# Performance work log

Hardware: AMD Instinct MI355X
Metric: run time of the kernel (lower is better)

The kernel has to match this reference:

```python
import jax, jax.numpy as jnp
import numpy as np
from jax import lax

HEADS = 8
DIM_HEAD = 8
SCALE = DIM_HEAD ** (-0.5)
UP = 64  # nn.Upsample(scale_factor=64), nearest


def _conv_s8(x, w, b):
    # Conv2d(inner, inner, 11x11, stride 8, padding 2) + exact GELU
    y = lax.conv_general_dilated(x, w, window_strides=(8, 8),
                                 padding=((2, 2), (2, 2)),
                                 dimension_numbers=('NCHW', 'OIHW', 'NCHW'))
    return jax.nn.gelu(y + b[None, :, None, None], approximate=False)


def setup_inputs() -> dict:
    key = jax.random.key(0)
    ks = jax.random.split(key, 8)
    b, c, h, w = 2, 64, 48, 48
    inner = HEADS * DIM_HEAD  # 64
    f = jax.random.normal(ks[0], (b, c, h, w), jnp.float32)
    w_qkv = jax.random.normal(ks[1], (inner * 3, c, 1, 1), jnp.float32) * 0.05
    wq = jax.random.normal(ks[2], (inner, inner, 11, 11), jnp.float32) * 0.02
    bq = jax.random.normal(ks[3], (inner,), jnp.float32) * 0.02
    wk = jax.random.normal(ks[4], (inner, inner, 11, 11), jnp.float32) * 0.02
    bk = jax.random.normal(ks[5], (inner,), jnp.float32) * 0.02
    pos_h = jax.random.normal(ks[6], (DIM_HEAD, h), jnp.float32) * SCALE
    pos_w = jax.random.normal(ks[7], (DIM_HEAD, w), jnp.float32) * SCALE
    return {"f": f, "w_qkv": w_qkv, "wq": wq, "bq": bq, "wk": wk,
            "bk": bk, "pos_h": pos_h, "pos_w": pos_w}


def reference(f, w_qkv, wq, bq, wk, bk, pos_h, pos_w):
    b, c, h, w = f.shape
    inner = HEADS * DIM_HEAD
    # 1x1 conv to qkv
    qkv = jnp.einsum('oc,bchw->bohw', w_qkv[:, :, 0, 0], f)
    q, k, v = jnp.split(qkv, 3, axis=1)  # each [b, inner, h, w]
    # positional logits from pre-conv q
    q_full = q.reshape(b, HEADS, DIM_HEAD, h * w)
    emb = (pos_h[:, :, None] + pos_w[:, None, :]).reshape(DIM_HEAD, h * w)
    pos_logits = jnp.einsum('bhci,cj->bhij', q_full, emb)  # [b,H,hw,hw]
    # strided conv + gelu on q,k
    qd = _conv_s8(q, wq, bq)
    kd = _conv_s8(k, wk, bk)
    m = qd.shape[-1]  # downsampled side
    qd = qd.reshape(b, HEADS, DIM_HEAD, m * m) * SCALE
    kd = kd.reshape(b, HEADS, DIM_HEAD, m * m)
    vv = v.reshape(b, HEADS, DIM_HEAD, h * w)
    dots = jnp.einsum('bhci,bhcj->bhij', qd, kd)  # [b,H,m^2,m^2]
    # nearest upsample x64 on last two dims
    dots = jnp.repeat(jnp.repeat(dots, UP, axis=-2), UP, axis=-1)
    attn = jax.nn.softmax(dots + pos_logits, axis=-1)
    fmap = jnp.einsum('bhij,bhcj->bhci', attn, vv)
    return fmap.reshape(b, inner, h, w)
```

## Files before the change

### kernel.cpp

```cpp
#include <hip/hip_runtime.h>
#include <math.h>

#define HW 2304
#define O192 192
#define SCALE_F 0.35355339059327373f

typedef unsigned int u32;
typedef __attribute__((address_space(1))) const u32 gu32;
typedef __attribute__((address_space(3))) u32 lu32;
__device__ __forceinline__ void dma16(const void* g, void* l) {
  __builtin_amdgcn_global_load_lds((gu32*)g, (lu32*)l, 16, 0, 0);
}

__global__ __launch_bounds__(256) void qkv_kernel(
    const float* __restrict__ F, const float* __restrict__ W,
    float* __restrict__ QKV, float* __restrict__ V2) {
  __shared__ __align__(16) float sW[384];
  int blk = blockIdx.x;
  int idx0 = blk * 256;
  int r0 = idx0 / HW;
  int r1 = (idx0 + 255) / HW;
  int tid = threadIdx.x;
  if (tid < 192) {
    int g = tid >> 6, c = tid & 63;
    sW[tid]       = W[((r0 & 63) + g * 64) * 64 + c];
    sW[192 + tid] = W[((r1 & 63) + g * 64) * 64 + c];
  }
  __syncthreads();
  int idx = idx0 + tid;
  int p  = idx % HW;
  int r  = idx / HW;
  int o0 = r & 63;
  int b  = r >> 6;
  const float4* w4 = (const float4*)(sW + ((r == r0) ? 0 : 192));
  const float* f = F + (b * 64) * HW + p;
  float aq = 0.f, ak = 0.f, av = 0.f;
  #pragma unroll 4
  for (int c4 = 0; c4 < 16; c4++) {
    float4 wq = w4[c4];
    float4 wk = w4[16 + c4];
    float4 wv = w4[32 + c4];
    float f0 = f[(c4 * 4 + 0) * HW];
    float f1 = f[(c4 * 4 + 1) * HW];
    float f2 = f[(c4 * 4 + 2) * HW];
    float f3 = f[(c4 * 4 + 3) * HW];
    aq = fmaf(wq.x, f0, aq); ak = fmaf(wk.x, f0, ak); av = fmaf(wv.x, f0, av);
    aq = fmaf(wq.y, f1, aq); ak = fmaf(wk.y, f1, ak); av = fmaf(wv.y, f1, av);
    aq = fmaf(wq.z, f2, aq); ak = fmaf(wk.z, f2, ak); av = fmaf(wv.z, f2, av);
    aq = fmaf(wq.w, f3, aq); ak = fmaf(wk.w, f3, ak); av = fmaf(wv.w, f3, av);
  }
  float* qp = QKV + (b * HW + p) * O192;
  qp[o0]      = aq;
  qp[o0 + 64] = ak;
  V2[(((b << 3) + (o0 >> 3)) * HW + p) * 8 + (o0 & 7)] = av;
}

__global__ __launch_bounds__(256) void conv_kernel(
    const float* __restrict__ QKV, const float* __restrict__ Wq,
    const float* __restrict__ Bq, const float* __restrict__ Wk,
    const float* __restrict__ Bk, float* __restrict__ QD) {
  __shared__ float sW[7744];
  __shared__ float sRed[4 * 64 * 6];
  int blk = blockIdx.x;
  int xcd = blk & 7;
  int T = xcd >> 2, b = (xcd >> 1) & 1, s = xcd & 1;
  int idx = (blk >> 3) * 2 + s;
  int o  = idx / 6;
  int oy = idx % 6;
  const float* Wg = T ? Wk : Wq;
  for (int i = threadIdx.x; i < 7744; i += 256) sW[i] = Wg[o * 7744 + i];
  __syncthreads();
  int wv = threadIdx.x >> 6;
  int c  = threadIdx.x & 63;
  const float* base = QKV + b * (HW * O192) + T * 64 + c;
  float acc[6];
  #pragma unroll
  for (int ox = 0; ox < 6; ox++) acc[ox] = 0.f;
  for (int kyi = 0; kyi < 3; kyi++) {
    int ky = wv * 3 + kyi;
    if (ky > 10) break;
    int y = oy * 8 - 2 + ky;
    if ((unsigned)y < 48u) {
      float xrow[48];
      #pragma unroll
      for (int x = 0; x < 48; x++) xrow[x] = base[(y * 48 + x) * O192];
      #pragma unroll
      for (int kx = 0; kx < 11; kx++) {
        float wt = sW[c * 121 + ky * 11 + kx];
        #pragma unroll
        for (int ox = 0; ox < 6; ox++) {
          int x = ox * 8 - 2 + kx;
          if (x >= 0 && x < 48) acc[ox] = fmaf(xrow[x], wt, acc[ox]);
        }
      }
    }
  }
  #pragma unroll
  for (int ox = 0; ox < 6; ox++) sRed[(wv * 64 + c) * 6 + ox] = acc[ox];
  __syncthreads();
  if (threadIdx.x < 64) {
    int t = threadIdx.x;
    float r[6];
    #pragma unroll
    for (int ox = 0; ox < 6; ox++)
      r[ox] = sRed[t * 6 + ox] + sRed[(64 + t) * 6 + ox]
            + sRed[(128 + t) * 6 + ox] + sRed[(192 + t) * 6 + ox];
    #pragma unroll
    for (int off = 32; off; off >>= 1) {
      #pragma unroll
      for (int ox = 0; ox < 6; ox++) r[ox] += __shfl_down(r[ox], off, 64);
    }
    if (t == 0) {
      float bias = T ? Bk[o] : Bq[o];
      #pragma unroll
      for (int ox = 0; ox < 6; ox++) {
        float g = r[ox] + bias;
        float ge = 0.5f * g * (1.0f + erff(g * 0.70710678118654752f));
        QD[((T * 2 + b) * 64 + o) * 36 + oy * 6 + ox] = ge;
      }
    }
  }
}

#define OFF_V    0
#define OFF_QLO  4608
#define OFF_QHI  5120
#define OFF_EA   5632
#define OFF_PHT  8704
#define OFF_PWT  8896
#define OFF_E    9280
#define OFF_Z    9352
#define SBUF_N   9384

__global__ __launch_bounds__(512) void attn_kernel(
    const float* __restrict__ QKV, const float* __restrict__ V2,
    const float* __restrict__ QD, const float* __restrict__ PH,
    const float* __restrict__ PW, float* __restrict__ Pnum,
    float* __restrict__ PZ) {
  __shared__ __align__(16) float sB[SBUF_N];
  int blk = blockIdx.x;
  int bh = blk & 15;
  int jh = (blk >> 4) & 1;
  int Ip = blk >> 5;
  int b = bh >> 3, h = bh & 7;
  int r0 = Ip * 128;
  int tid = threadIdx.x;
  int w = tid >> 6, lane = tid & 63;
  int l32 = lane & 31, chalf = lane >> 5;
  if (tid < 192) {
    sB[OFF_PHT + tid] = PH[(tid & 7) * 48 + jh * 24 + (tid >> 3)];
  } else {
    int i = tid - 192;
    sB[OFF_PWT + i] = PW[(i & 7) * 48 + (i >> 3)];
  }
  if (tid < 64) {
    int i = 320 + tid;
    sB[OFF_PWT + i] = PW[(i & 7) * 48 + (i >> 3)];
  }
  if (tid < 72) {
    int Ik = tid / 36, J = tid - Ik * 36;
    const float* qd = QD + ((0 + b) * 64 + h * 8) * 36 + (Ip * 2 + Ik);
    const float* kd = QD + ((2 + b) * 64 + h * 8) * 36 + J;
    float acc = 0.f;
    #pragma unroll
    for (int c8 = 0; c8 < 8; c8++) acc = fmaf(qd[c8 * 36], kd[c8 * 36], acc);
    sB[OFF_E + tid] = __expf(SCALE_F * acc);
  }
  if (tid < 256) {
    int row = tid >> 1, half = tid & 1;
    int slot = (row & 31) * 4 + (row >> 5);
    float4 qv = *(const float4*)(QKV + (b * HW + r0 + row) * O192 + h * 8 + half * 4);
    *(float4*)(sB + (half ? OFF_QHI : OFF_QLO) + slot * 4) = qv;
  }
  __syncthreads();
  #pragma unroll
  for (int m = 0; m < 6; m++) {
    int flat = tid + m * 512;
    int jyRel = flat >> 7, s = flat & 127;
    float4 qa = *(const float4*)(sB + OFF_QLO + s * 4);
    float4 qb = *(const float4*)(sB + OFF_QHI + s * 4);
    const float* pp = sB + OFF_PHT + jyRel * 8;
    float d = qa.x*pp[0]+qa.y*pp[1]+qa.z*pp[2]+qa.w*pp[3]
            + qb.x*pp[4]+qb.y*pp[5]+qb.z*pp[6]+qb.w*pp[7];
    sB[OFF_EA + flat] = __expf(d);
  }
  float eB[4][6];
  #pragma unroll
  for (int k8 = 0; k8 < 4; k8++) {
    float4 qa = *(const float4*)(sB + OFF_QLO + (l32 * 4 + k8) * 4);
    float4 qb = *(const float4*)(sB + OFF_QHI + (l32 * 4 + k8) * 4);
    #pragma unroll
    for (int i = 0; i < 6; i++) {
      const float* pp = sB + OFF_PWT + (w * 6 + i) * 8;
      float d = qa.x*pp[0]+qa.y*pp[1]+qa.z*pp[2]+qa.w*pp[3]
              + qb.x*pp[4]+qb.y*pp[5]+qb.z*pp[6]+qb.w*pp[7];
      eB[k8][i] = __expf(d);
    }
  }
  float accv[4][4], zz[4];
  #pragma unroll
  for (int k8 = 0; k8 < 4; k8++) {
    zz[k8] = 0.f;
    #pragma unroll
    for (int c = 0; c < 4; c++) accv[k8][c] = 0.f;
  }
  const float4* sV4 = (const float4*)(sB + OFF_V);
  for (int p = 0; p < 2; p++) {
    int pq = jh * 2 + p;
    __syncthreads();
    {
      const char* src = (const char*)(V2 + (size_t)bh * (HW * 8) + pq * 4608);
      for (int m = w; m < 18; m += 8)
        dma16(src + m * 1024 + lane * 16, (char*)(sB + OFF_V) + m * 1024);
    }
    __syncthreads();
    #pragma unroll
    for (int jyL = 0; jyL < 12; jyL++) {
      int jyRel = p * 12 + jyL;
      int jy = jh * 24 + jyRel;
      float4 ea = *(const float4*)(sB + OFF_EA + jyRel * 128 + l32 * 4);
      int cb = jy * 48 + w * 6;
      int J0 = cb >> 6, J1 = (cb + 5) >> 6;
      int ib = 64 - (cb & 63);
      float e00 = sB[OFF_E + J0], e01 = sB[OFF_E + 36 + J0];
      float e10 = sB[OFF_E + J1], e11 = sB[OFF_E + 36 + J1];
      float a0[4], a1[4];
      a0[0] = ea.x * e00; a0[1] = ea.y * e00;
      a0[2] = ea.z * e01; a0[3] = ea.w * e01;
      a1[0] = ea.x * e10; a1[1] = ea.y * e10;
      a1[2] = ea.z * e11; a1[3] = ea.w * e11;
      #pragma unroll
      for (int i = 0; i < 6; i++) {
        float4 v = sV4[(jyL * 48 + w * 6 + i) * 2 + chalf];
        bool s0 = (i < ib);
        #pragma unroll
        for (int k8 = 0; k8 < 4; k8++) {
          float wgt = (s0 ? a0[k8] : a1[k8]) * eB[k8][i];
          accv[k8][0] = fmaf(wgt, v.x, accv[k8][0]);
          accv[k8][1] = fmaf(wgt, v.y, accv[k8][1]);
          accv[k8][2] = fmaf(wgt, v.z, accv[k8][2]);
          accv[k8][3] = fmaf(wgt, v.w, accv[k8][3]);
          zz[k8] += wgt;
        }
      }
    }
  }
  float* sU = sB + OFF_EA;
  #pragma unroll
  for (int k8 = 0; k8 < 4; k8++) {
    __syncthreads();
    {
      float* rp = sU + (w * 64 + lane) * 5;
      rp[0] = accv[k8][0]; rp[1] = accv[k8][1];
      rp[2] = accv[k8][2]; rp[3] = accv[k8][3];
      rp[4] = zz[k8];
    }
    __syncthreads();
    if (tid < 256) {
      int row32 = tid & 31, c = tid >> 5;
      int ln = ((c >> 2) << 5) + row32;
      float num = 0.f;
      #pragma unroll
      for (int ww = 0; ww < 8; ww++) num += sU[(ww * 64 + ln) * 5 + (c & 3)];
      Pnum[((jh * 16 + bh) * 8 + c) * HW + r0 + k8 * 32 + row32] = num;
    } else if (tid < 288) {
      int row32 = tid & 31;
      float z = 0.f;
      #pragma unroll
      for (int ww = 0; ww < 8; ww++)
        z += sU[(ww * 64 + row32) * 5 + 4] + sU[(ww * 64 + 32 + row32) * 5 + 4];
      PZ[(jh * 16 + bh) * HW + r0 + k8 * 32 + row32] = z * 0.5f;
    }
  }
}

__global__ __launch_bounds__(256) void combine_kernel(
    const float* __restrict__ Pnum, const float* __restrict__ PZ,
    float* __restrict__ out) {
  int t = blockIdx.x * 256 + threadIdx.x;
  int row = t % HW;
  int rc = t / HW;
  int c = rc & 7, bh = rc >> 3;
  float num = Pnum[((bh) * 8 + c) * HW + row]
            + Pnum[((16 + bh) * 8 + c) * HW + row];
  float z = PZ[bh * HW + row] + PZ[(16 + bh) * HW + row];
  int b = bh >> 3, h = bh & 7;
  out[(b * 64 + h * 8 + c) * HW + row] = num / z;
}

extern "C" void kernel_launch(void* const* d_in, const int* in_sizes, int n_in,
                              void* d_out, int out_size, void* d_ws, size_t ws_size,
                              hipStream_t stream) {
  const float* F    = (const float*)d_in[0];
  const float* Wqkv = (const float*)d_in[1];
  const float* Wq   = (const float*)d_in[2];
  const float* Bq   = (const float*)d_in[3];
  const float* Wk   = (const float*)d_in[4];
  const float* Bk   = (const float*)d_in[5];
  const float* PH   = (const float*)d_in[6];
  const float* PW   = (const float*)d_in[7];
  float* out = (float*)d_out;

  float* ws   = (float*)d_ws;
  float* QKV  = ws;
  float* V2   = QKV + 2 * HW * O192;
  float* QD   = V2 + 2 * 8 * HW * 8;
  float* Pnum = QD + 2 * 2 * 64 * 36;
  float* PZ   = Pnum + 2 * 16 * 8 * HW;

  qkv_kernel    <<<1152, 256, 0, stream>>>(F, Wqkv, QKV, V2);
  conv_kernel   <<<1536, 256, 0, stream>>>(QKV, Wq, Bq, Wk, Bk, QD);
  attn_kernel   <<<576,  512, 0, stream>>>(QKV, V2, QD, PH, PW, Pnum, PZ);
  combine_kernel<<<1152, 256, 0, stream>>>(Pnum, PZ, out);
}
```

Measured before the change: 153.8 us.

## Specialize the single-segment inner loop and merge the epilogue into one reduction

The inner accumulation loop now takes a fast path when all six columns fall in the same upsampled block, skipping the second exponent load and the per-element select. The epilogue used to run four separate barrier-delimited reduction rounds. It now writes all accumulators at once into a larger shared buffer and reduces them in one pass. Launch bounds add a minimum-blocks hint of 6. The larger shared-memory footprint and the occupancy hint may raise register pressure or cut residency.

```diff
diff --git a/kernel.cpp b/kernel.cpp
--- a/kernel.cpp
+++ b/kernel.cpp
@@ -129,10 +129,9 @@
 #define OFF_PHT  8704
 #define OFF_PWT  8896
 #define OFF_E    9280
-#define OFF_Z    9352
-#define SBUF_N   9384
-
-__global__ __launch_bounds__(512) void attn_kernel(
+#define SBUF_N   10752
+
+__global__ __launch_bounds__(512, 6) void attn_kernel(
     const float* __restrict__ QKV, const float* __restrict__ V2,
     const float* __restrict__ QD, const float* __restrict__ PH,
     const float* __restrict__ PW, float* __restrict__ Pnum,
@@ -220,57 +219,82 @@
       int jy = jh * 24 + jyRel;
       float4 ea = *(const float4*)(sB + OFF_EA + jyRel * 128 + l32 * 4);
       int cb = jy * 48 + w * 6;
-      int J0 = cb >> 6, J1 = (cb + 5) >> 6;
       int ib = 64 - (cb & 63);
+      int J0 = cb >> 6;
       float e00 = sB[OFF_E + J0], e01 = sB[OFF_E + 36 + J0];
-      float e10 = sB[OFF_E + J1], e11 = sB[OFF_E + 36 + J1];
-      float a0[4], a1[4];
+      float a0[4];
       a0[0] = ea.x * e00; a0[1] = ea.y * e00;
       a0[2] = ea.z * e01; a0[3] = ea.w * e01;
-      a1[0] = ea.x * e10; a1[1] = ea.y * e10;
-      a1[2] = ea.z * e11; a1[3] = ea.w * e11;
-      #pragma unroll
-      for (int i = 0; i < 6; i++) {
-        float4 v = sV4[(jyL * 48 + w * 6 + i) * 2 + chalf];
-        bool s0 = (i < ib);
+      if (ib >= 6) {
         #pragma unroll
-        for (int k8 = 0; k8 < 4; k8++) {
-          float wgt = (s0 ? a0[k8] : a1[k8]) * eB[k8][i];
-          accv[k8][0] = fmaf(wgt, v.x, accv[k8][0]);
-          accv[k8][1] = fmaf(wgt, v.y, accv[k8][1]);
-          accv[k8][2] = fmaf(wgt, v.z, accv[k8][2]);
-          accv[k8][3] = fmaf(wgt, v.w, accv[k8][3]);
-          zz[k8] += wgt;
+        for (int i = 0; i < 6; i++) {
+          float4 v = sV4[(jyL * 48 + w * 6 + i) * 2 + chalf];
+          #pragma unroll
+          for (int k8 = 0; k8 < 4; k8++) {
+            float wgt = a0[k8] * eB[k8][i];
+            accv[k8][0] = fmaf(wgt, v.x, accv[k8][0]);
+            accv[k8][1] = fmaf(wgt, v.y, accv[k8][1]);
+            accv[k8][2] = fmaf(wgt, v.z, accv[k8][2]);
+            accv[k8][3] = fmaf(wgt, v.w, accv[k8][3]);
+            zz[k8] += wgt;
+          }
+        }
+      } else {
+        int J1 = (cb + 5) >> 6;
+        float e10 = sB[OFF_E + J1], e11 = sB[OFF_E + 36 + J1];
+        float a1[4];
+        a1[0] = ea.x * e10; a1[1] = ea.y * e10;
+        a1[2] = ea.z * e11; a1[3] = ea.w * e11;
+        #pragma unroll
+        for (int i = 0; i < 6; i++) {
+          float4 v = sV4[(jyL * 48 + w * 6 + i) * 2 + chalf];
+          bool s0 = (i < ib);
+          #pragma unroll
+          for (int k8 = 0; k8 < 4; k8++) {
+            float wgt = (s0 ? a0[k8] : a1[k8]) * eB[k8][i];
+            accv[k8][0] = fmaf(wgt, v.x, accv[k8][0]);
+            accv[k8][1] = fmaf(wgt, v.y, accv[k8][1]);
+            accv[k8][2] = fmaf(wgt, v.z, accv[k8][2]);
+            accv[k8][3] = fmaf(wgt, v.w, accv[k8][3]);
+            zz[k8] += wgt;
+          }
         }
       }
     }
   }
-  float* sU = sB + OFF_EA;
-  #pragma unroll
-  for (int k8 = 0; k8 < 4; k8++) {
-    __syncthreads();
-    {
-      float* rp = sU + (w * 64 + lane) * 5;
-      rp[0] = accv[k8][0]; rp[1] = accv[k8][1];
-      rp[2] = accv[k8][2]; rp[3] = accv[k8][3];
-      rp[4] = zz[k8];
-    }
-    __syncthreads();
-    if (tid < 256) {
-      int row32 = tid & 31, c = tid >> 5;
-      int ln = ((c >> 2) << 5) + row32;
-      float num = 0.f;
-      #pragma unroll
-      for (int ww = 0; ww < 8; ww++) num += sU[(ww * 64 + ln) * 5 + (c & 3)];
-      Pnum[((jh * 16 + bh) * 8 + c) * HW + r0 + k8 * 32 + row32] = num;
-    } else if (tid < 288) {
-      int row32 = tid & 31;
-      float z = 0.f;
-      #pragma unroll
-      for (int ww = 0; ww < 8; ww++)
-        z += sU[(ww * 64 + row32) * 5 + 4] + sU[(ww * 64 + 32 + row32) * 5 + 4];
-      PZ[(jh * 16 + bh) * HW + r0 + k8 * 32 + row32] = z * 0.5f;
-    }
+  __syncthreads();
+  {
+    float* rp = sB + (w * 64 + lane) * 21;
+    #pragma unroll
+    for (int k8 = 0; k8 < 4; k8++) {
+      rp[k8 * 4 + 0] = accv[k8][0];
+      rp[k8 * 4 + 1] = accv[k8][1];
+      rp[k8 * 4 + 2] = accv[k8][2];
+      rp[k8 * 4 + 3] = accv[k8][3];
+      rp[16 + k8]    = zz[k8];
+    }
+  }
+  __syncthreads();
+  if (tid < 128) {
+    int k8 = tid >> 5, r32 = tid & 31;
+    float z = 0.f;
+    #pragma unroll
+    for (int ww = 0; ww < 8; ww++)
+      z += sB[(ww * 64 + r32) * 21 + 16 + k8]
+         + sB[(ww * 64 + 32 + r32) * 21 + 16 + k8];
+    PZ[(jh * 16 + bh) * HW + r0 + tid] = z * 0.5f;
+  }
+  #pragma unroll
+  for (int cc0 = 0; cc0 < 2; cc0++) {
+    int cc = tid + cc0 * 512;
+    int row = cc & 127, c = cc >> 7;
+    int k8 = row >> 5, r32 = row & 31;
+    int ln = ((c >> 2) << 5) + r32;
+    float num = 0.f;
+    #pragma unroll
+    for (int ww = 0; ww < 8; ww++)
+      num += sB[(ww * 64 + ln) * 21 + k8 * 4 + (c & 3)];
+    Pnum[((jh * 16 + bh) * 8 + c) * HW + r0 + row] = num;
   }
 }
 
```

Measured after the change: 170.7 us. 10.9% more time.
